# Kernel optimization log

Hardware: AMD Instinct MI355X
Metric: run time of the kernel (lower is better)

The kernel has to match this reference:

```python
import jax, jax.numpy as jnp
import numpy as np

B, T, S, H, V, MAXL = 8, 128, 256, 1024, 32000, 512
STD = 0.02


def _ln(x, g, b):
    m = jnp.mean(x, -1, keepdims=True)
    v = jnp.mean((x - m) ** 2, -1, keepdims=True)
    return (x - m) / jnp.sqrt(v + 1e-5) * g + b


def setup_inputs() -> dict:
    key = jax.random.key(0)
    ks = jax.random.split(key, 16)
    n = lambda k, shape: jax.random.normal(k, shape, jnp.float32) * STD
    inp = {
        "input_ids": jax.random.randint(ks[0], (B, T), 0, V),
        "encoder_hidden_states": jax.random.normal(ks[1], (B, S, H), jnp.float32),
        "pattern_masks": jax.random.randint(ks[2], (B, T, V), 0, 2).astype(bool),
        "attention_mask": jnp.ones((B, S), bool),
        "tok_emb": n(ks[3], (V, H)),
        "pos_emb": n(ks[4], (MAXL, H)),
        "w_ih": n(ks[5], (4 * H, H)),
        "w_hh": n(ks[6], (4 * H, H)),
        "b_ih": jnp.zeros((4 * H,), jnp.float32),
        "b_hh": jnp.zeros((4 * H,), jnp.float32),
        "wq": n(ks[7], (H, H)), "bq": jnp.zeros((H,), jnp.float32),
        "wk": n(ks[8], (H, H)), "bk": jnp.zeros((H,), jnp.float32),
        "wc": n(ks[9], (H, 2 * H)), "bc": jnp.zeros((H,), jnp.float32),
        "wo": n(ks[10], (V, H)), "bo": jnp.zeros((V,), jnp.float32),
        "g1": n(ks[11], (H,)), "be1": jnp.zeros((H,), jnp.float32),
        "g2": n(ks[12], (H,)), "be2": jnp.zeros((H,), jnp.float32),
    }
    return inp


def reference(input_ids, encoder_hidden_states, pattern_masks, attention_mask,
              tok_emb, pos_emb, w_ih, w_hh, b_ih, b_hh,
              wq, bq, wk, bk, wc, bc, wo, bo, g1, be1, g2, be2):
    # Token + positional embedding (dropout is identity in eval)
    x = tok_emb[input_ids] + pos_emb[:T][None, :, :]  # [B,T,H]

    # Single-layer LSTM (PyTorch gate order i,f,g,o) via scan over time
    def step(carry, xt):
        h, c = carry
        gates = xt @ w_ih.T + b_ih + h @ w_hh.T + b_hh
        i, f, g, o = jnp.split(gates, 4, axis=-1)
        c = jax.nn.sigmoid(f) * c + jax.nn.sigmoid(i) * jnp.tanh(g)
        h = jax.nn.sigmoid(o) * jnp.tanh(c)
        return (h, c), h

    h0 = jnp.zeros((B, H), x.dtype)
    _, hs = jax.lax.scan(step, (h0, h0), jnp.swapaxes(x, 0, 1))
    lstm_out = jnp.swapaxes(hs, 0, 1)  # [B,T,H]

    # Attention: per-position loop in torch == batched over T (keys invariant)
    qn = _ln(lstm_out @ wq.T + bq, g1, be1)              # [B,T,H]
    kn = _ln(encoder_hidden_states @ wk.T + bk, g1, be1)  # [B,S,H]
    scale = H ** (-0.5) * 0.5
    scores = jnp.einsum('bth,bsh->bts', qn, kn) * scale
    am = attention_mask[:, None, :]
    scores = jnp.where(am, scores, -10000.0)
    mx = jnp.max(scores, -1, keepdims=True)
    ex = jnp.exp(scores - mx)
    ex = jnp.where(am, ex, 0.0)
    w = ex / (jnp.sum(ex, -1, keepdims=True) + 1e-6)
    ctx = jnp.einsum('bts,bsh->bth', w, kn)              # [B,T,H]

    hidden = _ln(jnp.concatenate([lstm_out, ctx], -1) @ wc.T + bc, g2, be2)
    logits = hidden @ wo.T + bo                           # [B,T,V]
    logits = jnp.where(pattern_masks, logits, -10000.0)
    return logits
```

## Files before the change

### kernel.cpp

```cpp
#include <hip/hip_runtime.h>
#include <cstdint>
#include <cstddef>

#define Bdim 8
#define Tdim 128
#define Sdim 256
#define Hdim 1024
#define Vdim 32000
#define SENT 0xFFFFFFFFFFFFFFFFULL

typedef unsigned short u16;
typedef unsigned long long u64;
typedef __attribute__((ext_vector_type(8))) short short8;
typedef __attribute__((ext_vector_type(4))) short short4v;
typedef __attribute__((ext_vector_type(4))) float f32x4;
typedef __attribute__((ext_vector_type(2))) unsigned long long u64x2;

union Frag { short8 v; short4v h[2]; };

__device__ __forceinline__ float bf2f(u16 u){
  union { unsigned int i; float f; } x; x.i = ((unsigned int)u) << 16; return x.f;
}
__device__ __forceinline__ u16 f2b(float f){
  union { float f; unsigned int u; } x; x.f = f;
  unsigned int r = x.u + 0x7FFFu + ((x.u >> 16) & 1u);
  return (u16)(r >> 16);
}
__device__ __forceinline__ float ftanh(float x){
  x = fminf(10.f, fmaxf(-10.f, x));
  const float e = __expf(2.f * x);
  return (e - 1.f) / (e + 1.f);
}

__device__ __forceinline__ void gload16(const void* g, void* l){
  __builtin_amdgcn_global_load_lds((const __attribute__((address_space(1))) unsigned int*)g,
                                   (__attribute__((address_space(3))) unsigned int*)l, 16, 0, 0);
}

__device__ __forceinline__ int qsw(int r){ return (r + (r >> 2)) & 3; }

__device__ __forceinline__ u64 aload(const u64* p){
  return __hip_atomic_load(p, __ATOMIC_RELAXED, __HIP_MEMORY_SCOPE_AGENT);
}
__device__ __forceinline__ void astore(u64* p, u64 v){
  __hip_atomic_store(p, v, __ATOMIC_RELAXED, __HIP_MEMORY_SCOPE_AGENT);
}

__device__ __forceinline__ bool mask_at(const void* m, size_t idx, int byteflag){
  if (byteflag) return ((const unsigned char*)m)[idx] != 0;
  return ((const int*)m)[idx] != 0;
}

template<typename OutT, bool BF32, int MASK, int NT>
__device__ __forceinline__ void gemm_core(
    char* ldsA0, char* ldsB0, char* ldsA1, char* ldsB1,
    int m0, int n0, int z,
    const u16* __restrict__ A, int lda, long sA,
    const void* __restrict__ Bp, int ldb, long sB,
    OutT* __restrict__ C, int ldc, long sC,
    const float* __restrict__ bias,
    const void* __restrict__ mask,
    const int* __restrict__ mflag,
    int K, float alpha)
{
  const int tid  = threadIdx.x;
  const int lane = tid & 63, wid = tid >> 6;
  const int lm = lane & 15, lg = lane >> 4;
  const int wm = wid >> 1, wn = wid & 1;
  const char* Ab = (const char*)(A + (size_t)z * sA);

  f32x4 acc[4][4 * NT];
#pragma unroll
  for (int i = 0; i < 4; i++)
#pragma unroll
    for (int j = 0; j < 4 * NT; j++) acc[i][j] = (f32x4){0.f, 0.f, 0.f, 0.f};

  const int brow = tid >> 1, bhalf = tid & 1;
  const int qb_st = qsw(brow);

  auto stageA = [&](char* dst, int k0){
    const char* ga = Ab + ((size_t)m0 * lda + k0) * 2;
    const int f0 = tid, f1 = tid + 256;
    const int r0 = f0 >> 2, r1 = f1 >> 2;
    gload16(ga + (size_t)r0 * (lda * 2) + ((f0 & 3) ^ qsw(r0)) * 16, dst + (f0 & ~63) * 16);
    gload16(ga + (size_t)r1 * (lda * 2) + ((f1 & 3) ^ qsw(r1)) * 16, dst + (f1 & ~63) * 16);
  };
  auto stageB16 = [&](char* dst, int k0){
    const char* gbase = (const char*)((const u16*)Bp + (size_t)z * sB);
#pragma unroll
    for (int s = 0; s < NT; s++) {
      const char* gb = gbase + ((size_t)(n0 + s * 128) * ldb + k0) * 2;
      const int f0 = tid, f1 = tid + 256;
      const int r0 = f0 >> 2, r1 = f1 >> 2;
      gload16(gb + (size_t)r0 * (ldb * 2) + ((f0 & 3) ^ qsw(r0)) * 16, dst + s * 8192 + (f0 & ~63) * 16);
      gload16(gb + (size_t)r1 * (ldb * 2) + ((f1 & 3) ^ qsw(r1)) * 16, dst + s * 8192 + (f1 & ~63) * 16);
    }
  };

  float4 nv0, nv1, nv2, nv3;
  auto loadB32 = [&](int k0){
    const float* Bf = (const float*)Bp + (size_t)z * sB;
    const float4* src = (const float4*)(Bf + (size_t)(n0 + brow) * ldb + k0 + bhalf * 16);
    nv0 = src[0]; nv1 = src[1]; nv2 = src[2]; nv3 = src[3];
  };
  auto writeB32 = [&](char* dst){
    union { short8 v; short s[8]; } p0, p1;
    p0.s[0]=(short)f2b(nv0.x); p0.s[1]=(short)f2b(nv0.y); p0.s[2]=(short)f2b(nv0.z); p0.s[3]=(short)f2b(nv0.w);
    p0.s[4]=(short)f2b(nv1.x); p0.s[5]=(short)f2b(nv1.y); p0.s[6]=(short)f2b(nv1.z); p0.s[7]=(short)f2b(nv1.w);
    p1.s[0]=(short)f2b(nv2.x); p1.s[1]=(short)f2b(nv2.y); p1.s[2]=(short)f2b(nv2.z); p1.s[3]=(short)f2b(nv2.w);
    p1.s[4]=(short)f2b(nv3.x); p1.s[5]=(short)f2b(nv3.y); p1.s[6]=(short)f2b(nv3.z); p1.s[7]=(short)f2b(nv3.w);
    char* base = dst + brow * 64;
    *(short8*)(base + (((bhalf * 2 + 0) ^ qb_st) * 16)) = p0.v;
    *(short8*)(base + (((bhalf * 2 + 1) ^ qb_st) * 16)) = p1.v;
  };

  stageA(ldsA0, 0);
  if (BF32) { loadB32(0); writeB32(ldsB0); }
  else stageB16(ldsB0, 0);
  __syncthreads();

  char *cA = ldsA0, *cB = ldsB0, *nA = ldsA1, *nB = ldsB1;
  const int nk = K >> 5;
  for (int i = 0; i < nk; i++) {
    const bool more = (i + 1) < nk;
    if (more) {
      stageA(nA, (i + 1) << 5);
      if (BF32) loadB32((i + 1) << 5);
      else stageB16(nB, (i + 1) << 5);
    }
    Frag a[4];
#pragma unroll
    for (int mi = 0; mi < 4; mi++) {
      const int rr = wm * 64 + mi * 16 + lm;
      const int q = qsw(rr);
      const char* p = cA + rr * 64 + (lg & 1) * 8;
      a[mi].h[0] = *(const short4v*)(p + (((lg >> 1) ^ q) * 16));
      a[mi].h[1] = *(const short4v*)(p + ((((lg >> 1) | 2) ^ q) * 16));
    }
#pragma unroll
    for (int ni = 0; ni < 4 * NT; ni++) {
      const int s = ni >> 2, nl = ni & 3;
      const int rr = wn * 64 + nl * 16 + lm;
      const int q = qsw(rr);
      const char* p = cB + s * 8192 + rr * 64 + (lg & 1) * 8;
      Frag b;
      b.h[0] = *(const short4v*)(p + (((lg >> 1) ^ q) * 16));
      b.h[1] = *(const short4v*)(p + ((((lg >> 1) | 2) ^ q) * 16));
#pragma unroll
      for (int mi = 0; mi < 4; mi++)
        acc[mi][ni] = __builtin_amdgcn_mfma_f32_16x16x32_bf16(a[mi].v, b.v, acc[mi][ni], 0, 0, 0);
    }
    if (BF32 && more) writeB32(nB);
    __syncthreads();
    char* t;
    t = cA; cA = nA; nA = t;
    t = cB; cB = nB; nB = t;
  }

  const int bflag = (MASK == 1) ? *mflag : 0;
#pragma unroll
  for (int mi = 0; mi < 4; mi++) {
#pragma unroll
    for (int ni = 0; ni < 4 * NT; ni++) {
      const int row = m0 + wm * 64 + mi * 16 + lg * 4;
      const int col = n0 + (ni >> 2) * 128 + wn * 64 + (ni & 3) * 16 + lm;
      const float bb = bias ? bias[col] : 0.f;
#pragma unroll
      for (int j = 0; j < 4; j++) {
        float v = acc[mi][ni][j] * alpha + bb;
        const size_t midx = (size_t)(row + j) * ldc + col;
        if (MASK == 1) { if (!mask_at(mask, midx, bflag)) v = -10000.0f; }
        if (MASK == 2) { if (!((const unsigned char*)mask)[midx]) v = -10000.0f; }
        const size_t o = (size_t)z * sC + midx;
        if constexpr (sizeof(OutT) == 2) C[o] = (OutT)f2b(v); else C[o] = (OutT)v;
      }
    }
  }
}

template<typename OutT, bool BF32, int MASK, bool SWAP, int NT = 1>
__global__ __launch_bounds__(256) void gemm_bt(
    const u16* __restrict__ A, int lda, long sA,
    const void* __restrict__ Bp, int ldb, long sB,
    OutT* __restrict__ C, int ldc, long sC,
    const float* __restrict__ bias,
    const void* __restrict__ mask,
    const int* __restrict__ mflag,
    int K, float alpha)
{
  __shared__ alignas(16) char lds[(8192 + 8192 * NT) * 2];
  const int m0 = (SWAP ? blockIdx.x : blockIdx.y) * 128;
  const int n0 = (SWAP ? blockIdx.y : blockIdx.x) * (128 * NT);
  char* ldsA1 = lds + 8192 + 8192 * NT;
  gemm_core<OutT, BF32, MASK, NT>(lds, lds + 8192, ldsA1, ldsA1 + 8192,
      m0, n0, blockIdx.z, A, lda, sA, Bp, ldb, sB, C, ldc, sC,
      bias, mask, mflag, K, alpha);
}

__device__ void lstm_body(char* smem,
    const u16* __restrict__ xpre, const u16* __restrict__ whh,
    u16* __restrict__ hbuf, u16* __restrict__ cat, int bx)
{
  u16* wlds = (u16*)smem;
  u16* hlds = (u16*)(smem + 131072);
  const int tid = threadIdx.x, lane = tid & 63, wid = tid >> 6;
  const int lm = lane & 15, lg = lane >> 4;
  const int gcol0 = bx * 64;

  for (int q = tid; q < 8192; q += 256) {
    const int r = q >> 7, cc = q & 127;
    gload16(whh + (size_t)(gcol0 + r) * 1024 + (size_t)(cc ^ (r & 7)) * 8,
            (char*)wlds + (q & ~63) * 16);
  }

  float c_reg = 0.f;
  const int rloc = wid * 16 + lm, swb = rloc & 7, swa = lm & 7;
  const u16* wl = wlds + rloc * 1024;
  const u16* hl = hlds + swa * 1024;
  const int pk = tid >> 2, qq = tid & 3;
  const u16* xp = xpre + (size_t)(lm * Tdim) * 4096 + gcol0 + wid * 16 + lg * 4;

  for (int t = 0; t < Tdim; t++) {
    u64 xw = 0;
    if (lm < 8) xw = *(const u64*)(xp + (size_t)t * 4096);
    if (t > 0) {
      const u64* ps = (const u64*)(hbuf + ((size_t)(t - 1) * 64 + pk) * 128) + qq * 8;
      u64 w0=SENT,w1=SENT,w2=SENT,w3=SENT,w4=SENT,w5=SENT,w6=SENT,w7=SENT;
      for (;;) {
        if (w0 == SENT) w0 = aload(ps + 0);
        if (w1 == SENT) w1 = aload(ps + 1);
        if (w2 == SENT) w2 = aload(ps + 2);
        if (w3 == SENT) w3 = aload(ps + 3);
        if (w4 == SENT) w4 = aload(ps + 4);
        if (w5 == SENT) w5 = aload(ps + 5);
        if (w6 == SENT) w6 = aload(ps + 6);
        if (w7 == SENT) w7 = aload(ps + 7);
        if (w0 != SENT && w1 != SENT && w2 != SENT && w3 != SENT &&
            w4 != SENT && w5 != SENT && w6 != SENT && w7 != SENT) break;
        __builtin_amdgcn_s_sleep(1);
      }
      {
        const int m = qq * 2;
        u64x2 a; a[0] = w0; a[1] = w1;
        u64x2 b; b[0] = w2; b[1] = w3;
        *(u64x2*)((char*)hlds + m * 2048 + (((pk * 2 + 0) ^ m) * 16)) = a;
        *(u64x2*)((char*)hlds + m * 2048 + (((pk * 2 + 1) ^ m) * 16)) = b;
      }
      {
        const int m = qq * 2 + 1;
        u64x2 a; a[0] = w4; a[1] = w5;
        u64x2 b; b[0] = w6; b[1] = w7;
        *(u64x2*)((char*)hlds + m * 2048 + (((pk * 2 + 0) ^ m) * 16)) = a;
        *(u64x2*)((char*)hlds + m * 2048 + (((pk * 2 + 1) ^ m) * 16)) = b;
      }
    }
    __syncthreads();

    f32x4 acc0, acc1, acc2, acc3;
    {
      union { u64 w; u16 s[4]; } xu; xu.w = xw;
      acc0[0] = bf2f(xu.s[0]); acc0[1] = bf2f(xu.s[1]);
      acc0[2] = bf2f(xu.s[2]); acc0[3] = bf2f(xu.s[3]);
    }
    acc1 = (f32x4){0.f,0.f,0.f,0.f};
    acc2 = (f32x4){0.f,0.f,0.f,0.f};
    acc3 = (f32x4){0.f,0.f,0.f,0.f};

    if (t > 0) {
#pragma unroll
      for (int kk = 0; kk < 32; kk++) {
        const int c0 = kk * 4 + (lg >> 1);
        const int sub = (lg & 1) * 4;
        Frag aw, bh;
        aw.h[0] = *(const short4v*)(wl + ((c0 ^ swb) << 3) + sub);
        aw.h[1] = *(const short4v*)(wl + (((c0 + 2) ^ swb) << 3) + sub);
        bh.h[0] = *(const short4v*)(hl + ((c0 ^ swa) << 3) + sub);
        bh.h[1] = *(const short4v*)(hl + (((c0 + 2) ^ swa) << 3) + sub);
        if ((kk & 3) == 0)      acc0 = __builtin_amdgcn_mfma_f32_16x16x32_bf16(aw.v, bh.v, acc0, 0, 0, 0);
        else if ((kk & 3) == 1) acc1 = __builtin_amdgcn_mfma_f32_16x16x32_bf16(aw.v, bh.v, acc1, 0, 0, 0);
        else if ((kk & 3) == 2) acc2 = __builtin_amdgcn_mfma_f32_16x16x32_bf16(aw.v, bh.v, acc2, 0, 0, 0);
        else                    acc3 = __builtin_amdgcn_mfma_f32_16x16x32_bf16(aw.v, bh.v, acc3, 0, 0, 0);
      }
    }
    const f32x4 g4 = (acc0 + acc1) + (acc2 + acc3);

    const float si = 1.f / (1.f + __expf(-g4[0]));
    const float sf = 1.f / (1.f + __expf(-g4[1]));
    const float so = 1.f / (1.f + __expf(-g4[3]));
    const float cn = sf * c_reg + si * ftanh(g4[2]);
    c_reg = cn;
    const float hn = so * ftanh(cn);
    const int hb = (int)f2b(hn);

    const int v0 = __shfl(hb, lm, 64);
    const int v1 = __shfl(hb, lm + 16, 64);
    const int v2 = __shfl(hb, lm + 32, 64);
    const int v3 = __shfl(hb, lm + 48, 64);
    if (lg == 0 && lm < 8) {
      const u64 pack = (u64)(v0 & 0xFFFF) | ((u64)(v1 & 0xFFFF) << 16)
                     | ((u64)(v2 & 0xFFFF) << 32) | ((u64)(v3 & 0xFFFF) << 48);
      astore((u64*)(hbuf + ((size_t)t * 64 + bx) * 128 + lm * 16 + wid * 4), pack);
      *(u64*)(cat + (size_t)(lm * Tdim + t) * 2048 + bx * 16 + wid * 4) = pack;
    }
    __syncthreads();
  }
}

__global__ __launch_bounds__(256) void lstm_plus(
    const u16* __restrict__ xpre, const u16* __restrict__ whh,
    u16* __restrict__ hbuf, u16* __restrict__ cat,
    const u16* __restrict__ encb, const u16* __restrict__ wkb,
    float* __restrict__ klin, const float* __restrict__ bk,
    const float* __restrict__ wo, u16* __restrict__ wob,
    const float* __restrict__ wq, u16* __restrict__ wqb,
    const float* __restrict__ wc, u16* __restrict__ wcb,
    const void* __restrict__ pmask, unsigned char* __restrict__ pmaskb,
    const int* __restrict__ bflag)
{
  __shared__ alignas(16) char smem[147456];
  const int bx = blockIdx.x;
  if (bx < 64) {
    lstm_body(smem, xpre, whh, hbuf, cat, bx);
  } else if (bx < 192) {
    const int idx = bx - 64;
    gemm_core<float, false, 0, 1>(smem, smem + 8192, smem + 16384, smem + 24576,
        (idx >> 3) * 128, (idx & 7) * 128, 0,
        encb, 1024, 0, wkb, 1024, 0, klin, 1024, 0, bk, nullptr, nullptr, 1024, 1.f);
  } else {
    const int s = bx - 192;
    const int tid = threadIdx.x;
    for (int r = s; r < 1024; r += 64) {
      const size_t i = (size_t)r * 1024 + tid * 4;
      const float4 v = *(const float4*)(wq + i);
      u16* op = wqb + i;
      op[0] = f2b(v.x); op[1] = f2b(v.y); op[2] = f2b(v.z); op[3] = f2b(v.w);
    }
    for (int r = s; r < 1024; r += 64) {
#pragma unroll
      for (int hc = 0; hc < 2; hc++) {
        const size_t i = (size_t)r * 2048 + hc * 1024 + tid * 4;
        const float4 v = *(const float4*)(wc + i);
        u16* op = wcb + i;
        op[0] = f2b(v.x); op[1] = f2b(v.y); op[2] = f2b(v.z); op[3] = f2b(v.w);
      }
    }
    if (wob) {
      for (int r = s; r < Vdim; r += 64) {
        const size_t i = (size_t)r * 1024 + tid * 4;
        const float4 v = *(const float4*)(wo + i);
        u16* op = wob + i;
        op[0] = f2b(v.x); op[1] = f2b(v.y); op[2] = f2b(v.z); op[3] = f2b(v.w);
      }
    }
    if (pmaskb) {
      const int bfl = *bflag;
      const size_t total = (size_t)Bdim * Tdim * Vdim;
      const size_t nthr = 64 * 256;
      if (bfl == 0) {
        for (size_t i = ((size_t)s * 256 + tid) * 4; i < total; i += nthr * 4) {
          const int4 v = *(const int4*)((const int*)pmask + i);
          uchar4 o;
          o.x = v.x ? 1 : 0; o.y = v.y ? 1 : 0; o.z = v.z ? 1 : 0; o.w = v.w ? 1 : 0;
          *(uchar4*)(pmaskb + i) = o;
        }
      } else {
        for (size_t i = ((size_t)s * 256 + tid) * 16; i < total; i += nthr * 16) {
          *(int4*)(pmaskb + i) = *(const int4*)((const unsigned char*)pmask + i);
        }
      }
    }
  }
}

__global__ __launch_bounds__(256) void prep_k(
    const float* __restrict__ w_hh, const float* __restrict__ w_ih,
    const float* __restrict__ wk,   const float* __restrict__ enc,
    const int* __restrict__ ids,
    const float* __restrict__ tok,  const float* __restrict__ pos,
    const float* __restrict__ b_ih, const float* __restrict__ b_hh,
    const unsigned char* __restrict__ pmask,
    u16* __restrict__ whhb, u16* __restrict__ wihb, u16* __restrict__ wkb,
    u16* __restrict__ encb, u16* __restrict__ xbf,
    float* __restrict__ biasf, u64* __restrict__ hbuf, int* __restrict__ bflag)
{
  __shared__ int sdet;
  const int b = blockIdx.x, tid = threadIdx.x;
  if (b < 8192) {
    const bool ih = b >= 4096;
    const int r = b & 4095;
    const int p = (r & 3) * Hdim + (r >> 2);
    const float4 v = *(const float4*)((ih ? w_ih : w_hh) + (size_t)p * Hdim + tid * 4);
    u16* op = (ih ? wihb : whhb) + (size_t)r * Hdim + tid * 4;
    op[0] = f2b(v.x); op[1] = f2b(v.y); op[2] = f2b(v.z); op[3] = f2b(v.w);
  } else if (b < 9216) {
    const size_t i = (size_t)(b - 8192) * 1024 + tid * 4;
    const float4 v = *(const float4*)(wk + i);
    u16* op = wkb + i;
    op[0] = f2b(v.x); op[1] = f2b(v.y); op[2] = f2b(v.z); op[3] = f2b(v.w);
  } else if (b < 11264) {
    const size_t i = (size_t)(b - 9216) * 1024 + tid * 4;
    const float4 v = *(const float4*)(enc + i);
    u16* op = encb + i;
    op[0] = f2b(v.x); op[1] = f2b(v.y); op[2] = f2b(v.z); op[3] = f2b(v.w);
  } else if (b < 12288) {
    const int row = b - 11264;
    const int t = row & (Tdim - 1);
    const int id = ids[row];
    const int h0 = tid * 4;
    const float4 a = *(const float4*)(tok + (size_t)id * Hdim + h0);
    const float4 p = *(const float4*)(pos + (size_t)t * Hdim + h0);
    u16* op = xbf + (size_t)row * Hdim + h0;
    op[0] = f2b(a.x + p.x); op[1] = f2b(a.y + p.y); op[2] = f2b(a.z + p.z); op[3] = f2b(a.w + p.w);
  } else if (b < 12292) {
    const int n0 = (b - 12288) * 1024 + tid * 4;
#pragma unroll
    for (int j = 0; j < 4; j++) {
      const int n = n0 + j;
      const int p = (n & 3) * Hdim + (n >> 2);
      biasf[n] = b_ih[p] + b_hh[p];
    }
  } else if (b < 12548) {
    const size_t i = ((size_t)(b - 12292) * 256 + tid) * 4;
    u64x2 s2; s2[0] = SENT; s2[1] = SENT;
    *(u64x2*)(hbuf + i)     = s2;
    *(u64x2*)(hbuf + i + 2) = s2;
  } else {
    if (tid == 0) sdet = 0;
    __syncthreads();
    int loc = 0;
    for (int i = tid; i < 65536; i += 256)
      if ((i & 3) && pmask[i]) loc = 1;
    if (loc) atomicOr(&sdet, 1);
    __syncthreads();
    if (tid == 0) bflag[0] = sdet;
  }
}

__global__ __launch_bounds__(256) void ln_rows(const float* __restrict__ in, u16* __restrict__ out,
                                               const float* __restrict__ g, const float* __restrict__ be){
  const int row = blockIdx.x, tid = threadIdx.x;
  const int lane = tid & 63, wid = tid >> 6;
  const float4 x = *(const float4*)(in + (size_t)row * Hdim + tid * 4);
  float s = x.x + x.y + x.z + x.w;
  float q = x.x * x.x + x.y * x.y + x.z * x.z + x.w * x.w;
  for (int o = 32; o; o >>= 1) { s += __shfl_down(s, o, 64); q += __shfl_down(q, o, 64); }
  __shared__ float sm[8];
  if (lane == 0) { sm[wid] = s; sm[4 + wid] = q; }
  __syncthreads();
  const float ts = sm[0] + sm[1] + sm[2] + sm[3];
  const float tq = sm[4] + sm[5] + sm[6] + sm[7];
  const float mean = ts * (1.f / Hdim);
  const float var  = tq * (1.f / Hdim) - mean * mean;
  const float r = rsqrtf(var + 1e-5f);
  const int h0 = tid * 4;
  const float4 gv = *(const float4*)(g + h0);
  const float4 bv = *(const float4*)(be + h0);
  u16* op = out + (size_t)row * Hdim + h0;
  op[0] = f2b((x.x - mean) * r * gv.x + bv.x);
  op[1] = f2b((x.y - mean) * r * gv.y + bv.y);
  op[2] = f2b((x.z - mean) * r * gv.z + bv.z);
  op[3] = f2b((x.w - mean) * r * gv.w + bv.w);
}
__global__ __launch_bounds__(256) void softmax_k(const float* __restrict__ sc, const void* __restrict__ am,
                                                 const int* __restrict__ mflag, u16* __restrict__ w){
  const int row = blockIdx.x, tid = threadIdx.x;
  const int lane = tid & 63, wid = tid >> 6;
  const int b = row >> 7;
  const int bflag = *mflag;
  const float v = sc[(size_t)row * Sdim + tid];
  const bool mk = mask_at(am, (size_t)b * Sdim + tid, bflag);
  const float vm = mk ? v : -10000.0f;
  float mx = vm;
  for (int o = 32; o; o >>= 1) mx = fmaxf(mx, __shfl_down(mx, o, 64));
  __shared__ float sm[8];
  if (lane == 0) sm[wid] = mx;
  __syncthreads();
  mx = fmaxf(fmaxf(sm[0], sm[1]), fmaxf(sm[2], sm[3]));
  const float ex = mk ? expf(vm - mx) : 0.f;
  float ss = ex;
  for (int o = 32; o; o >>= 1) ss += __shfl_down(ss, o, 64);
  if (lane == 0) sm[4 + wid] = ss;
  __syncthreads();
  const float tot = sm[4] + sm[5] + sm[6] + sm[7];
  w[(size_t)row * Sdim + tid] = f2b(ex / (tot + 1e-6f));
}
__global__ __launch_bounds__(256) void transp_k(const u16* __restrict__ kn, u16* __restrict__ knT){
  __shared__ u16 tile[64][65];
  const int b = blockIdx.z, h0 = blockIdx.x * 64, s0 = blockIdx.y * 64;
  const u16* src = kn  + (size_t)b * Sdim * Hdim;
  u16* dst       = knT + (size_t)b * Hdim * Sdim;
  for (int e = threadIdx.x; e < 4096; e += 256) {
    const int r = e >> 6, c = e & 63;
    tile[r][c] = src[(size_t)(s0 + r) * Hdim + h0 + c];
  }
  __syncthreads();
  for (int e = threadIdx.x; e < 4096; e += 256) {
    const int hr = e >> 6, scc = e & 63;
    dst[(size_t)(h0 + hr) * Sdim + s0 + scc] = tile[scc][hr];
  }
}

extern "C" void kernel_launch(void* const* d_in, const int* in_sizes, int n_in,
                              void* d_out, int out_size, void* d_ws, size_t ws_size,
                              hipStream_t stream) {
  const int*   input_ids = (const int*)d_in[0];
  const float* enc   = (const float*)d_in[1];
  const void*  pmask = d_in[2];
  const void*  amask = d_in[3];
  const float* tok  = (const float*)d_in[4];
  const float* pos  = (const float*)d_in[5];
  const float* w_ih = (const float*)d_in[6];
  const float* w_hh = (const float*)d_in[7];
  const float* b_ih = (const float*)d_in[8];
  const float* b_hh = (const float*)d_in[9];
  const float* wq = (const float*)d_in[10];
  const float* bq = (const float*)d_in[11];
  const float* wk = (const float*)d_in[12];
  const float* bk = (const float*)d_in[13];
  const float* wc = (const float*)d_in[14];
  const float* bc = (const float*)d_in[15];
  const float* wo = (const float*)d_in[16];
  const float* bo = (const float*)d_in[17];
  const float* g1  = (const float*)d_in[18];
  const float* be1 = (const float*)d_in[19];
  const float* g2  = (const float*)d_in[20];
  const float* be2 = (const float*)d_in[21];
  float* out = (float*)d_out;

  char* ws = (char*)d_ws;
  size_t off = 0;
  auto alloc = [&](size_t b){ size_t o = off; off += (b + 255) & ~(size_t)255; return o; };
  u16*   whhb  = (u16*)  (ws + alloc((size_t)4096 * 1024 * 2));
  u16*   wihb  = (u16*)  (ws + alloc((size_t)4096 * 1024 * 2));
  u16*   wqb   = (u16*)  (ws + alloc((size_t)1024 * 1024 * 2));
  u16*   wkb   = (u16*)  (ws + alloc((size_t)1024 * 1024 * 2));
  u16*   wcb   = (u16*)  (ws + alloc((size_t)1024 * 2048 * 2));
  float* biasf = (float*)(ws + alloc(4096 * 4));
  u16*   xbf   = (u16*)  (ws + alloc((size_t)1024 * 1024 * 2));
  u16*   encb  = (u16*)  (ws + alloc((size_t)2048 * 1024 * 2));
  u16*   xpre  = (u16*)  (ws + alloc((size_t)1024 * 4096 * 2));
  u16*   hbuf  = (u16*)  (ws + alloc((size_t)Tdim * 64 * 128 * 2));
  u16*   cat   = (u16*)  (ws + alloc((size_t)1024 * 2048 * 2));
  float* qlin  = (float*)(ws + alloc((size_t)1024 * 1024 * 4));
  u16*   qn    = (u16*)  (ws + alloc((size_t)1024 * 1024 * 2));
  float* klin  = (float*)(ws + alloc((size_t)2048 * 1024 * 4));
  u16*   kn    = (u16*)  (ws + alloc((size_t)2048 * 1024 * 2));
  u16*   knT   = (u16*)  (ws + alloc((size_t)2048 * 1024 * 2));
  float* scores= (float*)(ws + alloc((size_t)8 * 128 * 256 * 4));
  u16*   attw  = (u16*)  (ws + alloc((size_t)8 * 128 * 256 * 2));
  float* hlin  = (float*)(ws + alloc((size_t)1024 * 1024 * 4));
  u16*   hid   = (u16*)  (ws + alloc((size_t)1024 * 1024 * 2));
  int*   bflag = (int*)  (ws + alloc(256));
  unsigned char* pmaskb = (unsigned char*)(ws + alloc((size_t)Bdim * Tdim * Vdim));
  const bool havePak = off <= ws_size;
  u16*   wob   = (u16*)  (ws + alloc((size_t)Vdim * Hdim * 2));
  const bool haveWob = off <= ws_size;
  if (!havePak) pmaskb = nullptr;
  if (!haveWob) wob = nullptr;
  (void)in_sizes; (void)n_in; (void)out_size;

  prep_k<<<12549, 256, 0, stream>>>(w_hh, w_ih, wk, enc, input_ids,
      tok, pos, b_ih, b_hh, (const unsigned char*)pmask,
      whhb, wihb, wkb, encb, xbf, biasf, (u64*)hbuf, bflag);

  gemm_bt<u16, false, 0, false><<<dim3(32, 8, 1), 256, 0, stream>>>(
      xbf, 1024, 0, wihb, 1024, 0, xpre, 4096, 0, biasf, nullptr, nullptr, 1024, 1.f);

  lstm_plus<<<256, 256, 0, stream>>>(xpre, whhb, hbuf, cat, encb, wkb, klin, bk,
                                     wo, wob, wq, wqb, wc, wcb, pmask, pmaskb, bflag);

  gemm_bt<float, false, 0, false><<<dim3(8, 8, 1), 256, 0, stream>>>(
      cat, 2048, 0, wqb, 1024, 0, qlin, 1024, 0, bq, nullptr, nullptr, 1024, 1.f);
  ln_rows<<<1024, 256, 0, stream>>>(qlin, qn, g1, be1);
  ln_rows<<<2048, 256, 0, stream>>>(klin, kn, g1, be1);
  transp_k<<<dim3(16, 4, 8), 256, 0, stream>>>(kn, knT);

  gemm_bt<float, false, 0, false><<<dim3(2, 1, 8), 256, 0, stream>>>(
      qn, 1024, 131072, kn, 1024, 262144, scores, 256, 32768, nullptr, nullptr, nullptr, 1024, 0.015625f);
  softmax_k<<<1024, 256, 0, stream>>>(scores, amask, bflag, attw);
  gemm_bt<u16, false, 0, false><<<dim3(8, 1, 8), 256, 0, stream>>>(
      attw, 256, 32768, knT, 256, 262144, cat + 1024, 2048, 262144, nullptr, nullptr, nullptr, 256, 1.f);

  gemm_bt<float, false, 0, false><<<dim3(8, 8, 1), 256, 0, stream>>>(
      cat, 2048, 0, wcb, 2048, 0, hlin, 1024, 0, bc, nullptr, nullptr, 2048, 1.f);
  ln_rows<<<1024, 256, 0, stream>>>(hlin, hid, g2, be2);

  if (wob && pmaskb)
    gemm_bt<float, false, 2, true><<<dim3(8, 250, 1), 256, 0, stream>>>(
        hid, 1024, 0, wob, 1024, 0, out, 32000, 0, bo, pmaskb, nullptr, 1024, 1.f);
  else if (wob)
    gemm_bt<float, false, 1, true><<<dim3(8, 250, 1), 256, 0, stream>>>(
        hid, 1024, 0, wob, 1024, 0, out, 32000, 0, bo, pmask, bflag, 1024, 1.f);
  else
    gemm_bt<float, true, 1, true><<<dim3(8, 250, 1), 256, 0, stream>>>(
        hid, 1024, 0, wo, 1024, 0, out, 32000, 0, bo, pmask, bflag, 1024, 1.f);
}
```

Before: 800.6 us.

## Split-K score GEMM, fuse LayerNorm launches, XCD-swizzle output GEMM, drop NT tiling

The attention score GEMM becomes a split-K kernel over four K chunks that accumulate with atomicAdd into a scores buffer zeroed inside the prep kernel. This raises block count for a GEMM that previously launched only 16 blocks. The q and k LayerNorm launches are merged into one kernel. The vocab projection GEMM gets a block-index remap that groups tiles by XCD for L2 locality, and the unused NT wide-tile template parameter is removed. Atomic accumulation adds contention and makes the summation order nondeterministic.

```diff
diff --git a/kernel.cpp b/kernel.cpp
--- a/kernel.cpp
+++ b/kernel.cpp
@@ -51,7 +51,7 @@
   return ((const int*)m)[idx] != 0;
 }
 
-template<typename OutT, bool BF32, int MASK, int NT>
+template<typename OutT, bool BF32, int MASK, bool ATOMIC = false>
 __device__ __forceinline__ void gemm_core(
     char* ldsA0, char* ldsB0, char* ldsA1, char* ldsB1,
     int m0, int n0, int z,
@@ -69,11 +69,11 @@
   const int wm = wid >> 1, wn = wid & 1;
   const char* Ab = (const char*)(A + (size_t)z * sA);
 
-  f32x4 acc[4][4 * NT];
+  f32x4 acc[4][4];
 #pragma unroll
   for (int i = 0; i < 4; i++)
 #pragma unroll
-    for (int j = 0; j < 4 * NT; j++) acc[i][j] = (f32x4){0.f, 0.f, 0.f, 0.f};
+    for (int j = 0; j < 4; j++) acc[i][j] = (f32x4){0.f, 0.f, 0.f, 0.f};
 
   const int brow = tid >> 1, bhalf = tid & 1;
   const int qb_st = qsw(brow);
@@ -86,15 +86,11 @@
     gload16(ga + (size_t)r1 * (lda * 2) + ((f1 & 3) ^ qsw(r1)) * 16, dst + (f1 & ~63) * 16);
   };
   auto stageB16 = [&](char* dst, int k0){
-    const char* gbase = (const char*)((const u16*)Bp + (size_t)z * sB);
-#pragma unroll
-    for (int s = 0; s < NT; s++) {
-      const char* gb = gbase + ((size_t)(n0 + s * 128) * ldb + k0) * 2;
-      const int f0 = tid, f1 = tid + 256;
-      const int r0 = f0 >> 2, r1 = f1 >> 2;
-      gload16(gb + (size_t)r0 * (ldb * 2) + ((f0 & 3) ^ qsw(r0)) * 16, dst + s * 8192 + (f0 & ~63) * 16);
-      gload16(gb + (size_t)r1 * (ldb * 2) + ((f1 & 3) ^ qsw(r1)) * 16, dst + s * 8192 + (f1 & ~63) * 16);
-    }
+    const char* gb = (const char*)((const u16*)Bp + (size_t)z * sB) + ((size_t)n0 * ldb + k0) * 2;
+    const int f0 = tid, f1 = tid + 256;
+    const int r0 = f0 >> 2, r1 = f1 >> 2;
+    gload16(gb + (size_t)r0 * (ldb * 2) + ((f0 & 3) ^ qsw(r0)) * 16, dst + (f0 & ~63) * 16);
+    gload16(gb + (size_t)r1 * (ldb * 2) + ((f1 & 3) ^ qsw(r1)) * 16, dst + (f1 & ~63) * 16);
   };
 
   float4 nv0, nv1, nv2, nv3;
@@ -138,11 +134,10 @@
       a[mi].h[1] = *(const short4v*)(p + ((((lg >> 1) | 2) ^ q) * 16));
     }
 #pragma unroll
-    for (int ni = 0; ni < 4 * NT; ni++) {
-      const int s = ni >> 2, nl = ni & 3;
-      const int rr = wn * 64 + nl * 16 + lm;
+    for (int ni = 0; ni < 4; ni++) {
+      const int rr = wn * 64 + ni * 16 + lm;
       const int q = qsw(rr);
-      const char* p = cB + s * 8192 + rr * 64 + (lg & 1) * 8;
+      const char* p = cB + rr * 64 + (lg & 1) * 8;
       Frag b;
       b.h[0] = *(const short4v*)(p + (((lg >> 1) ^ q) * 16));
       b.h[1] = *(const short4v*)(p + ((((lg >> 1) | 2) ^ q) * 16));
@@ -161,9 +156,9 @@
 #pragma unroll
   for (int mi = 0; mi < 4; mi++) {
 #pragma unroll
-    for (int ni = 0; ni < 4 * NT; ni++) {
+    for (int ni = 0; ni < 4; ni++) {
       const int row = m0 + wm * 64 + mi * 16 + lg * 4;
-      const int col = n0 + (ni >> 2) * 128 + wn * 64 + (ni & 3) * 16 + lm;
+      const int col = n0 + wn * 64 + ni * 16 + lm;
       const float bb = bias ? bias[col] : 0.f;
 #pragma unroll
       for (int j = 0; j < 4; j++) {
@@ -172,13 +167,17 @@
         if (MASK == 1) { if (!mask_at(mask, midx, bflag)) v = -10000.0f; }
         if (MASK == 2) { if (!((const unsigned char*)mask)[midx]) v = -10000.0f; }
         const size_t o = (size_t)z * sC + midx;
-        if constexpr (sizeof(OutT) == 2) C[o] = (OutT)f2b(v); else C[o] = (OutT)v;
-      }
-    }
-  }
-}
-
-template<typename OutT, bool BF32, int MASK, bool SWAP, int NT = 1>
+        if constexpr (ATOMIC) {
+          atomicAdd((float*)&C[o], v);
+        } else {
+          if constexpr (sizeof(OutT) == 2) C[o] = (OutT)f2b(v); else C[o] = (OutT)v;
+        }
+      }
+    }
+  }
+}
+
+template<typename OutT, bool BF32, int MASK, bool SWAP, bool XSWZ = false>
 __global__ __launch_bounds__(256) void gemm_bt(
     const u16* __restrict__ A, int lda, long sA,
     const void* __restrict__ Bp, int ldb, long sB,
@@ -188,13 +187,34 @@
     const int* __restrict__ mflag,
     int K, float alpha)
 {
-  __shared__ alignas(16) char lds[(8192 + 8192 * NT) * 2];
-  const int m0 = (SWAP ? blockIdx.x : blockIdx.y) * 128;
-  const int n0 = (SWAP ? blockIdx.y : blockIdx.x) * (128 * NT);
-  char* ldsA1 = lds + 8192 + 8192 * NT;
-  gemm_core<OutT, BF32, MASK, NT>(lds, lds + 8192, ldsA1, ldsA1 + 8192,
+  __shared__ alignas(16) char lds[32768];
+  int m0, n0;
+  if (XSWZ) {
+    const int bid = blockIdx.x + gridDim.x * blockIdx.y;
+    const int per = (gridDim.x * gridDim.y) >> 3;
+    const int L = (bid & 7) * per + (bid >> 3);
+    m0 = (L % gridDim.x) * 128;
+    n0 = (L / gridDim.x) * 128;
+  } else {
+    m0 = (SWAP ? blockIdx.x : blockIdx.y) * 128;
+    n0 = (SWAP ? blockIdx.y : blockIdx.x) * 128;
+  }
+  gemm_core<OutT, BF32, MASK>(lds, lds + 8192, lds + 16384, lds + 24576,
       m0, n0, blockIdx.z, A, lda, sA, Bp, ldb, sB, C, ldc, sC,
       bias, mask, mflag, K, alpha);
+}
+
+__global__ __launch_bounds__(256) void gemm_sk(
+    const u16* __restrict__ A, int lda, long sA,
+    const u16* __restrict__ Bt, int ldb, long sB,
+    float* __restrict__ C, int ldc, long sC, float alpha)
+{
+  __shared__ alignas(16) char lds[32768];
+  const int kc = blockIdx.y;
+  gemm_core<float, false, 0, true>(lds, lds + 8192, lds + 16384, lds + 24576,
+      0, blockIdx.x * 128, blockIdx.z,
+      A + kc * 256, lda, sA, Bt + kc * 256, ldb, sB,
+      C, ldc, sC, nullptr, nullptr, nullptr, 256, alpha);
 }
 
 __device__ void lstm_body(char* smem,
@@ -323,7 +343,7 @@
     lstm_body(smem, xpre, whh, hbuf, cat, bx);
   } else if (bx < 192) {
     const int idx = bx - 64;
-    gemm_core<float, false, 0, 1>(smem, smem + 8192, smem + 16384, smem + 24576,
+    gemm_core<float, false, 0>(smem, smem + 8192, smem + 16384, smem + 24576,
         (idx >> 3) * 128, (idx & 7) * 128, 0,
         encb, 1024, 0, wkb, 1024, 0, klin, 1024, 0, bk, nullptr, nullptr, 1024, 1.f);
   } else {
@@ -381,7 +401,8 @@
     const unsigned char* __restrict__ pmask,
     u16* __restrict__ whhb, u16* __restrict__ wihb, u16* __restrict__ wkb,
     u16* __restrict__ encb, u16* __restrict__ xbf,
-    float* __restrict__ biasf, u64* __restrict__ hbuf, int* __restrict__ bflag)
+    float* __restrict__ biasf, u64* __restrict__ hbuf,
+    float* __restrict__ scores, int* __restrict__ bflag)
 {
   __shared__ int sdet;
   const int b = blockIdx.x, tid = threadIdx.x;
@@ -424,6 +445,10 @@
     u64x2 s2; s2[0] = SENT; s2[1] = SENT;
     *(u64x2*)(hbuf + i)     = s2;
     *(u64x2*)(hbuf + i + 2) = s2;
+  } else if (b < 12804) {
+    const size_t i = ((size_t)(b - 12548) * 256 + tid) * 4;
+    float4 z; z.x = 0.f; z.y = 0.f; z.z = 0.f; z.w = 0.f;
+    *(float4*)(scores + i) = z;
   } else {
     if (tid == 0) sdet = 0;
     __syncthreads();
@@ -436,9 +461,10 @@
   }
 }
 
-__global__ __launch_bounds__(256) void ln_rows(const float* __restrict__ in, u16* __restrict__ out,
-                                               const float* __restrict__ g, const float* __restrict__ be){
-  const int row = blockIdx.x, tid = threadIdx.x;
+__device__ __forceinline__ void ln_row_body(const float* __restrict__ in, u16* __restrict__ out,
+                                            int row, const float* __restrict__ g,
+                                            const float* __restrict__ be){
+  const int tid = threadIdx.x;
   const int lane = tid & 63, wid = tid >> 6;
   const float4 x = *(const float4*)(in + (size_t)row * Hdim + tid * 4);
   float s = x.x + x.y + x.z + x.w;
@@ -460,6 +486,17 @@
   op[1] = f2b((x.y - mean) * r * gv.y + bv.y);
   op[2] = f2b((x.z - mean) * r * gv.z + bv.z);
   op[3] = f2b((x.w - mean) * r * gv.w + bv.w);
+}
+__global__ __launch_bounds__(256) void ln_rows(const float* __restrict__ in, u16* __restrict__ out,
+                                               const float* __restrict__ g, const float* __restrict__ be){
+  ln_row_body(in, out, blockIdx.x, g, be);
+}
+__global__ __launch_bounds__(256) void ln_qk(const float* __restrict__ qlin, u16* __restrict__ qn,
+                                             const float* __restrict__ klin, u16* __restrict__ kn,
+                                             const float* __restrict__ g, const float* __restrict__ be){
+  const int row = blockIdx.x;
+  if (row < 1024) ln_row_body(qlin, qn, row, g, be);
+  else            ln_row_body(klin, kn, row - 1024, g, be);
 }
 __global__ __launch_bounds__(256) void softmax_k(const float* __restrict__ sc, const void* __restrict__ am,
                                                  const int* __restrict__ mflag, u16* __restrict__ w){
@@ -559,9 +596,9 @@
   if (!haveWob) wob = nullptr;
   (void)in_sizes; (void)n_in; (void)out_size;
 
-  prep_k<<<12549, 256, 0, stream>>>(w_hh, w_ih, wk, enc, input_ids,
+  prep_k<<<12805, 256, 0, stream>>>(w_hh, w_ih, wk, enc, input_ids,
       tok, pos, b_ih, b_hh, (const unsigned char*)pmask,
-      whhb, wihb, wkb, encb, xbf, biasf, (u64*)hbuf, bflag);
+      whhb, wihb, wkb, encb, xbf, biasf, (u64*)hbuf, scores, bflag);
 
   gemm_bt<u16, false, 0, false><<<dim3(32, 8, 1), 256, 0, stream>>>(
       xbf, 1024, 0, wihb, 1024, 0, xpre, 4096, 0, biasf, nullptr, nullptr, 1024, 1.f);
@@ -571,12 +608,11 @@
 
   gemm_bt<float, false, 0, false><<<dim3(8, 8, 1), 256, 0, stream>>>(
       cat, 2048, 0, wqb, 1024, 0, qlin, 1024, 0, bq, nullptr, nullptr, 1024, 1.f);
-  ln_rows<<<1024, 256, 0, stream>>>(qlin, qn, g1, be1);
-  ln_rows<<<2048, 256, 0, stream>>>(klin, kn, g1, be1);
+  ln_qk<<<3072, 256, 0, stream>>>(qlin, qn, klin, kn, g1, be1);
   transp_k<<<dim3(16, 4, 8), 256, 0, stream>>>(kn, knT);
 
-  gemm_bt<float, false, 0, false><<<dim3(2, 1, 8), 256, 0, stream>>>(
-      qn, 1024, 131072, kn, 1024, 262144, scores, 256, 32768, nullptr, nullptr, nullptr, 1024, 0.015625f);
+  gemm_sk<<<dim3(2, 4, 8), 256, 0, stream>>>(
+      qn, 1024, 131072, kn, 1024, 262144, scores, 256, 32768, 0.015625f);
   softmax_k<<<1024, 256, 0, stream>>>(scores, amask, bflag, attw);
   gemm_bt<u16, false, 0, false><<<dim3(8, 1, 8), 256, 0, stream>>>(
       attw, 256, 32768, knT, 256, 262144, cat + 1024, 2048, 262144, nullptr, nullptr, nullptr, 256, 1.f);
@@ -586,7 +622,7 @@
   ln_rows<<<1024, 256, 0, stream>>>(hlin, hid, g2, be2);
 
   if (wob && pmaskb)
-    gemm_bt<float, false, 2, true><<<dim3(8, 250, 1), 256, 0, stream>>>(
+    gemm_bt<float, false, 2, false, true><<<dim3(8, 250, 1), 256, 0, stream>>>(
         hid, 1024, 0, wob, 1024, 0, out, 32000, 0, bo, pmaskb, nullptr, 1024, 1.f);
   else if (wob)
     gemm_bt<float, false, 1, true><<<dim3(8, 250, 1), 256, 0, stream>>>(
```

After: 777.8 us. 2.9% less time.
